# Optimization experiments

Hardware: AMD Instinct MI355X
Metric: run time of the kernel (lower is better)

## Reference

```python
import jax, jax.numpy as jnp
import numpy as np

N, IN_DIM, HIDDEN, OUT_DIM = 16384, 4, 64, 2


def setup_inputs() -> dict:
    key = jax.random.key(0)
    ks = jax.random.split(key, 12)
    x = jax.random.normal(ks[0], (N, IN_DIM), dtype=jnp.float32)
    adj = jax.random.uniform(ks[1], (N, N), dtype=jnp.float32)
    adj = adj / jnp.sum(adj, axis=1, keepdims=True)  # row-normalised
    s = 0.1
    return {
        "x": x,
        "adj": adj,
        # msg_mlp: Linear(4,64) -> Tanh -> Linear(64,64)
        "W1": jax.random.normal(ks[2], (IN_DIM, HIDDEN), dtype=jnp.float32) * s,
        "b1": jnp.zeros((HIDDEN,), dtype=jnp.float32),
        "W2": jax.random.normal(ks[3], (HIDDEN, HIDDEN), dtype=jnp.float32) * s,
        "b2": jnp.zeros((HIDDEN,), dtype=jnp.float32),
        # update_mlp: Linear(68,64) -> Tanh -> Linear(64,64) -> Tanh
        "U1": jax.random.normal(ks[4], (IN_DIM + HIDDEN, HIDDEN), dtype=jnp.float32) * s,
        "c1": jnp.zeros((HIDDEN,), dtype=jnp.float32),
        "U2": jax.random.normal(ks[5], (HIDDEN, HIDDEN), dtype=jnp.float32) * s,
        "c2": jnp.zeros((HIDDEN,), dtype=jnp.float32),
        # out_head: Linear(64,2)
        "Wo": jax.random.normal(ks[6], (HIDDEN, OUT_DIM), dtype=jnp.float32) * s,
        "bo": jnp.zeros((OUT_DIM,), dtype=jnp.float32),
    }


def reference(x, adj, W1, b1, W2, b2, U1, c1, U2, c2, Wo, bo):
    # messages = msg_mlp(x): (N, HIDDEN)
    messages = jnp.tanh(x @ W1 + b1) @ W2 + b2
    # aggregate over neighbours: (N,N) @ (N,HIDDEN)
    agg = adj @ messages
    # combined = [x, agg]: (N, IN_DIM+HIDDEN)
    combined = jnp.concatenate([x, agg], axis=-1)
    h = jnp.tanh(jnp.tanh(combined @ U1 + c1) @ U2 + c2)
    acc = h @ Wo + bo  # (N, OUT_DIM)
    return acc
```

## Files before the change

### kernel.cpp

```cpp
#include <hip/hip_runtime.h>
#include <math.h>

#define NN 16384
#define IN_DIM 4
#define HID 64
#define OUT_DIM 2
#define BK 256
#define NT (NN / BK)

typedef __bf16 bf16x8 __attribute__((ext_vector_type(8)));
typedef float  f32x4  __attribute__((ext_vector_type(4)));

__device__ __forceinline__ void gload_lds16(const float* g, void* lds) {
    __builtin_amdgcn_global_load_lds(
        (const __attribute__((address_space(1))) void*)g,
        (__attribute__((address_space(3))) void*)lds, 16, 0, 0);
}

template<int N> __device__ __forceinline__ void waitv() {
    asm volatile("s_waitcnt vmcnt(%0)" :: "n"(N) : "memory");
    __builtin_amdgcn_sched_barrier(0);
}

__global__ __launch_bounds__(256) void k_messages(
    const float* __restrict__ x, const float* __restrict__ W1,
    const float* __restrict__ b1, const float* __restrict__ W2,
    const float* __restrict__ b2, __bf16* __restrict__ msgT)
{
    __shared__ float  xs[64 * 4];
    __shared__ float  h1[64 * 64];
    __shared__ __bf16 mt[64 * 66];

    const int t = threadIdx.x;
    const int node0 = blockIdx.x * 64;
    xs[t] = x[node0 * 4 + t];
    __syncthreads();

    const int h = t & 63, g = t >> 6;
    for (int n = g * 16; n < g * 16 + 16; ++n) {
        float acc = b1[h];
        #pragma unroll
        for (int k = 0; k < 4; ++k) acc += xs[n * 4 + k] * W1[k * 64 + h];
        h1[n * 64 + h] = tanhf(acc);
    }
    __syncthreads();
    for (int n = g * 16; n < g * 16 + 16; ++n) {
        float acc = b2[h];
        #pragma unroll 8
        for (int k = 0; k < 64; ++k) acc += h1[n * 64 + k] * W2[k * 64 + h];
        mt[h * 66 + n] = (__bf16)acc;
    }
    __syncthreads();
    for (int slot = t; slot < 512; slot += 256) {
        const int r = slot >> 3, c = (slot & 7) * 8;
        bf16x8 v;
        #pragma unroll
        for (int j = 0; j < 8; ++j) v[j] = mt[r * 66 + c + j];
        *(bf16x8*)(msgT + (size_t)r * NN + node0 + c) = v;
    }
}

__global__ __launch_bounds__(128, 1) void k_agg(
    const float* __restrict__ adj, const __bf16* __restrict__ msgT,
    float* __restrict__ agg)
{
    __shared__ float As[2][2][16 * BK];

    const int t = threadIdx.x;
    const int wave = t >> 6, lane = t & 63;
    const int m0 = blockIdx.x * 32 + wave * 16;
    const int r15 = lane & 15;
    const int kg  = lane >> 4;

    const float*  arow  = adj  + (size_t)m0 * NN;
    const __bf16* bbase = msgT + (size_t)r15 * NN + kg * 8;

    float* wbuf0 = &As[0][wave][0];
    float* wbuf1 = &As[1][wave][0];

    f32x4 acc0 = {}, acc1 = {}, acc2 = {}, acc3 = {};
    bf16x8 bc0, bc1, bc2, bc3, bn0, bn1, bn2, bn3;

    #pragma unroll
    for (int g = 0; g < 16; ++g)
        gload_lds16(arow + (size_t)g * NN + ((lane ^ g) << 2), wbuf0 + g * BK);
    bc0 = *(const bf16x8*)(bbase);
    bc1 = *(const bf16x8*)(bbase + 16 * (size_t)NN);
    bc2 = *(const bf16x8*)(bbase + 32 * (size_t)NN);
    bc3 = *(const bf16x8*)(bbase + 48 * (size_t)NN);

#define KSTEP(KT, KK, WAITN, DOSTAGE, DOBN)                                        \
    {                                                                              \
        if (DOBN) {                                                                \
            const int nkt = ((KK) == 7) ? (KT) + 1 : (KT);                         \
            const int nkk = ((KK) + 1) & 7;                                        \
            const __bf16* bp = bbase + (size_t)nkt * BK + nkk * 32;                \
            bn0 = *(const bf16x8*)(bp);                                            \
            bn1 = *(const bf16x8*)(bp + 16 * (size_t)NN);                          \
            bn2 = *(const bf16x8*)(bp + 32 * (size_t)NN);                          \
            bn3 = *(const bf16x8*)(bp + 48 * (size_t)NN);                          \
        }                                                                          \
        if (WAITN) waitv<(WAITN) ? (WAITN) : 63>();                                \
        const float* Ab = (((KT) & 1) ? wbuf1 : wbuf0) + r15 * BK;                 \
        f32x4 alo = *(const f32x4*)(Ab + ((((KK) * 8 + kg * 2 + 0) ^ r15) << 2));  \
        f32x4 ahi = *(const f32x4*)(Ab + ((((KK) * 8 + kg * 2 + 1) ^ r15) << 2));  \
        bf16x8 af;                                                                 \
        af[0] = (__bf16)alo[0]; af[1] = (__bf16)alo[1];                            \
        af[2] = (__bf16)alo[2]; af[3] = (__bf16)alo[3];                            \
        af[4] = (__bf16)ahi[0]; af[5] = (__bf16)ahi[1];                            \
        af[6] = (__bf16)ahi[2]; af[7] = (__bf16)ahi[3];                            \
        acc0 = __builtin_amdgcn_mfma_f32_16x16x32_bf16(af, bc0, acc0, 0, 0, 0);    \
        acc1 = __builtin_amdgcn_mfma_f32_16x16x32_bf16(af, bc1, acc1, 0, 0, 0);    \
        acc2 = __builtin_amdgcn_mfma_f32_16x16x32_bf16(af, bc2, acc2, 0, 0, 0);    \
        acc3 = __builtin_amdgcn_mfma_f32_16x16x32_bf16(af, bc3, acc3, 0, 0, 0);    \
        if (DOSTAGE) {                                                             \
            float* dst = (((KT) & 1) ? wbuf0 : wbuf1);                             \
            _Pragma("unroll")                                                      \
            for (int q = 0; q < 4; ++q) {                                          \
                const int g = (KK) * 4 + q;                                        \
                gload_lds16(arow + (size_t)g * NN + (size_t)((KT) + 1) * BK        \
                                 + ((lane ^ g) << 2), dst + g * BK);               \
            }                                                                      \
        }                                                                          \
        bc0 = bn0; bc1 = bn1; bc2 = bn2; bc3 = bn3;                                \
        __builtin_amdgcn_sched_barrier(0);                                         \
    }

    KSTEP(0, 0, 8, 1, 1);
    #pragma unroll
    for (int kk = 1; kk < 8; ++kk) KSTEP(0, kk, 0, (kk < 4), 1);

    for (int kt = 1; kt < NT - 1; ++kt) {
        KSTEP(kt, 0, 20, 1, 1);
        #pragma unroll
        for (int kk = 1; kk < 8; ++kk) KSTEP(kt, kk, 0, (kk < 4), 1);
    }

    KSTEP((NT - 1), 0, 20, 0, 1);
    #pragma unroll
    for (int kk = 1; kk < 8; ++kk) KSTEP((NT - 1), kk, 0, 0, (kk != 7));
#undef KSTEP

    const int rb = m0 + kg * 4;
    f32x4 accs[4] = {acc0, acc1, acc2, acc3};
    #pragma unroll
    for (int tt = 0; tt < 4; ++tt) {
        #pragma unroll
        for (int j = 0; j < 4; ++j) {
            agg[(size_t)(rb + j) * HID + tt * 16 + r15] = accs[tt][j];
        }
    }
}

__global__ __launch_bounds__(256) void k_update(
    const float* __restrict__ x, const float* __restrict__ agg,
    const float* __restrict__ U1, const float* __restrict__ c1,
    const float* __restrict__ U2, const float* __restrict__ c2,
    const float* __restrict__ Wo, const float* __restrict__ bo,
    float* __restrict__ out)
{
    __shared__ float comb[64 * 73];
    __shared__ float h1s[64 * 66];

    const int t = threadIdx.x, h = t & 63, g = t >> 6;
    const int node0 = blockIdx.x * 64;

    comb[(t >> 2) * 73 + (t & 3)] = x[node0 * 4 + t];
    for (int n = g * 16; n < g * 16 + 16; ++n) {
        comb[n * 73 + 4 + h] = agg[(size_t)(node0 + n) * HID + h];
    }
    __syncthreads();
    for (int n = g * 16; n < g * 16 + 16; ++n) {
        float acc = c1[h];
        #pragma unroll 4
        for (int k = 0; k < 68; ++k) acc += comb[n * 73 + k] * U1[k * 64 + h];
        h1s[n * 66 + h] = tanhf(acc);
    }
    __syncthreads();
    for (int n = g * 16; n < g * 16 + 16; ++n) {
        float acc = c2[h];
        #pragma unroll 8
        for (int k = 0; k < 64; ++k) acc += h1s[n * 66 + k] * U2[k * 64 + h];
        comb[n * 73 + h] = tanhf(acc);
    }
    __syncthreads();
    if (t < 128) {
        const int n = t >> 1, o = t & 1;
        float acc = bo[o];
        #pragma unroll 8
        for (int k = 0; k < 64; ++k) acc += comb[n * 73 + k] * Wo[k * 2 + o];
        out[(size_t)(node0 + n) * 2 + o] = acc;
    }
}

extern "C" void kernel_launch(void* const* d_in, const int* in_sizes, int n_in,
                              void* d_out, int out_size, void* d_ws, size_t ws_size,
                              hipStream_t stream)
{
    const float* x   = (const float*)d_in[0];
    const float* adj = (const float*)d_in[1];
    const float* W1  = (const float*)d_in[2];
    const float* b1  = (const float*)d_in[3];
    const float* W2  = (const float*)d_in[4];
    const float* b2  = (const float*)d_in[5];
    const float* U1  = (const float*)d_in[6];
    const float* c1  = (const float*)d_in[7];
    const float* U2  = (const float*)d_in[8];
    const float* c2  = (const float*)d_in[9];
    const float* Wo  = (const float*)d_in[10];
    const float* bo  = (const float*)d_in[11];
    float* out = (float*)d_out;

    __bf16* msgT = (__bf16*)d_ws;
    float*  agg  = (float*)((char*)d_ws + (size_t)HID * NN * sizeof(__bf16));

    k_messages<<<NN / 64, 256, 0, stream>>>(x, W1, b1, W2, b2, msgT);
    k_agg<<<NN / 32, 128, 0, stream>>>(adj, msgT, agg);
    k_update<<<NN / 64, 256, 0, stream>>>(x, agg, U1, c1, U2, c2, Wo, bo, out);
}
```

Measured before the change: 373.1 us.

## Process paired K-tiles per step and stagger each wave's starting tile

```diff
diff --git a/kernel.cpp b/kernel.cpp
--- a/kernel.cpp
+++ b/kernel.cpp
@@ -6,7 +6,7 @@
 #define HID 64
 #define OUT_DIM 2
 #define BK 256
-#define NT (NN / BK)
+#define NPAIR 32
 
 typedef __bf16 bf16x8 __attribute__((ext_vector_type(8)));
 typedef float  f32x4  __attribute__((ext_vector_type(4)));
@@ -64,81 +64,117 @@
     const float* __restrict__ adj, const __bf16* __restrict__ msgT,
     float* __restrict__ agg)
 {
-    __shared__ float As[2][2][16 * BK];
+    __shared__ float As[2][2][2][16 * BK];
 
     const int t = threadIdx.x;
     const int wave = t >> 6, lane = t & 63;
     const int m0 = blockIdx.x * 32 + wave * 16;
     const int r15 = lane & 15;
     const int kg  = lane >> 4;
+    const int phase = (blockIdx.x * 2 + wave) & (NPAIR - 1);
 
     const float*  arow  = adj  + (size_t)m0 * NN;
     const __bf16* bbase = msgT + (size_t)r15 * NN + kg * 8;
 
-    float* wbuf0 = &As[0][wave][0];
-    float* wbuf1 = &As[1][wave][0];
-
     f32x4 acc0 = {}, acc1 = {}, acc2 = {}, acc3 = {};
-    bf16x8 bc0, bc1, bc2, bc3, bn0, bn1, bn2, bn3;
-
-    #pragma unroll
-    for (int g = 0; g < 16; ++g)
-        gload_lds16(arow + (size_t)g * NN + ((lane ^ g) << 2), wbuf0 + g * BK);
-    bc0 = *(const bf16x8*)(bbase);
-    bc1 = *(const bf16x8*)(bbase + 16 * (size_t)NN);
-    bc2 = *(const bf16x8*)(bbase + 32 * (size_t)NN);
-    bc3 = *(const bf16x8*)(bbase + 48 * (size_t)NN);
-
-#define KSTEP(KT, KK, WAITN, DOSTAGE, DOBN)                                        \
+    bf16x8 bc0, bc1, bc2, bc3, bd0, bd1, bd2, bd3;
+    bf16x8 bn0, bn1, bn2, bn3, bn4, bn5, bn6, bn7;
+
+    {
+        const size_t c0 = (size_t)phase * BK;
+        const size_t c1 = c0 + NPAIR * BK;
+        float* d0 = &As[0][wave][0][0];
+        float* d1 = &As[0][wave][1][0];
+        #pragma unroll
+        for (int gp = 0; gp < 8; ++gp) {
+            const int g = gp * 2;
+            gload_lds16(arow + (size_t)g * NN + c0 + ((lane ^ g) << 2), d0 + g * BK);
+            gload_lds16(arow + (size_t)g * NN + c1 + ((lane ^ g) << 2), d1 + g * BK);
+            gload_lds16(arow + (size_t)(g + 1) * NN + c0 + ((lane ^ (g + 1)) << 2), d0 + (g + 1) * BK);
+            gload_lds16(arow + (size_t)(g + 1) * NN + c1 + ((lane ^ (g + 1)) << 2), d1 + (g + 1) * BK);
+        }
+        const __bf16* bp0 = bbase + (size_t)phase * BK;
+        const __bf16* bp1 = bp0 + (size_t)NPAIR * BK;
+        bc0 = *(const bf16x8*)(bp0);
+        bc1 = *(const bf16x8*)(bp0 + 16 * (size_t)NN);
+        bc2 = *(const bf16x8*)(bp0 + 32 * (size_t)NN);
+        bc3 = *(const bf16x8*)(bp0 + 48 * (size_t)NN);
+        bd0 = *(const bf16x8*)(bp1);
+        bd1 = *(const bf16x8*)(bp1 + 16 * (size_t)NN);
+        bd2 = *(const bf16x8*)(bp1 + 32 * (size_t)NN);
+        bd3 = *(const bf16x8*)(bp1 + 48 * (size_t)NN);
+    }
+
+#define KSTEP(KT, KK, GATE, DOSTAGE, DOBN)                                         \
     {                                                                              \
         if (DOBN) {                                                                \
             const int nkt = ((KK) == 7) ? (KT) + 1 : (KT);                         \
             const int nkk = ((KK) + 1) & 7;                                        \
-            const __bf16* bp = bbase + (size_t)nkt * BK + nkk * 32;                \
-            bn0 = *(const bf16x8*)(bp);                                            \
-            bn1 = *(const bf16x8*)(bp + 16 * (size_t)NN);                          \
-            bn2 = *(const bf16x8*)(bp + 32 * (size_t)NN);                          \
-            bn3 = *(const bf16x8*)(bp + 48 * (size_t)NN);                          \
+            const int npt = (nkt + phase) & (NPAIR - 1);                           \
+            const __bf16* bp0 = bbase + (size_t)npt * BK + nkk * 32;               \
+            const __bf16* bp1 = bp0 + (size_t)NPAIR * BK;                          \
+            bn0 = *(const bf16x8*)(bp0);                                           \
+            bn1 = *(const bf16x8*)(bp0 + 16 * (size_t)NN);                         \
+            bn2 = *(const bf16x8*)(bp0 + 32 * (size_t)NN);                         \
+            bn3 = *(const bf16x8*)(bp0 + 48 * (size_t)NN);                         \
+            bn4 = *(const bf16x8*)(bp1);                                           \
+            bn5 = *(const bf16x8*)(bp1 + 16 * (size_t)NN);                         \
+            bn6 = *(const bf16x8*)(bp1 + 32 * (size_t)NN);                         \
+            bn7 = *(const bf16x8*)(bp1 + 48 * (size_t)NN);                         \
         }                                                                          \
-        if (WAITN) waitv<(WAITN) ? (WAITN) : 63>();                                \
-        const float* Ab = (((KT) & 1) ? wbuf1 : wbuf0) + r15 * BK;                 \
-        f32x4 alo = *(const f32x4*)(Ab + ((((KK) * 8 + kg * 2 + 0) ^ r15) << 2));  \
-        f32x4 ahi = *(const f32x4*)(Ab + ((((KK) * 8 + kg * 2 + 1) ^ r15) << 2));  \
-        bf16x8 af;                                                                 \
-        af[0] = (__bf16)alo[0]; af[1] = (__bf16)alo[1];                            \
-        af[2] = (__bf16)alo[2]; af[3] = (__bf16)alo[3];                            \
-        af[4] = (__bf16)ahi[0]; af[5] = (__bf16)ahi[1];                            \
-        af[6] = (__bf16)ahi[2]; af[7] = (__bf16)ahi[3];                            \
-        acc0 = __builtin_amdgcn_mfma_f32_16x16x32_bf16(af, bc0, acc0, 0, 0, 0);    \
-        acc1 = __builtin_amdgcn_mfma_f32_16x16x32_bf16(af, bc1, acc1, 0, 0, 0);    \
-        acc2 = __builtin_amdgcn_mfma_f32_16x16x32_bf16(af, bc2, acc2, 0, 0, 0);    \
-        acc3 = __builtin_amdgcn_mfma_f32_16x16x32_bf16(af, bc3, acc3, 0, 0, 0);    \
+        if (GATE) waitv<8>();                                                      \
+        const float* A0 = &As[(KT) & 1][wave][0][0] + r15 * BK;                    \
+        const float* A1 = &As[(KT) & 1][wave][1][0] + r15 * BK;                    \
+        f32x4 alo0 = *(const f32x4*)(A0 + ((((KK) * 8 + kg * 2 + 0) ^ r15) << 2)); \
+        f32x4 ahi0 = *(const f32x4*)(A0 + ((((KK) * 8 + kg * 2 + 1) ^ r15) << 2)); \
+        f32x4 alo1 = *(const f32x4*)(A1 + ((((KK) * 8 + kg * 2 + 0) ^ r15) << 2)); \
+        f32x4 ahi1 = *(const f32x4*)(A1 + ((((KK) * 8 + kg * 2 + 1) ^ r15) << 2)); \
+        bf16x8 af0, af1;                                                           \
+        af0[0] = (__bf16)alo0[0]; af0[1] = (__bf16)alo0[1];                        \
+        af0[2] = (__bf16)alo0[2]; af0[3] = (__bf16)alo0[3];                        \
+        af0[4] = (__bf16)ahi0[0]; af0[5] = (__bf16)ahi0[1];                        \
+        af0[6] = (__bf16)ahi0[2]; af0[7] = (__bf16)ahi0[3];                        \
+        af1[0] = (__bf16)alo1[0]; af1[1] = (__bf16)alo1[1];                        \
+        af1[2] = (__bf16)alo1[2]; af1[3] = (__bf16)alo1[3];                        \
+        af1[4] = (__bf16)ahi1[0]; af1[5] = (__bf16)ahi1[1];                        \
+        af1[6] = (__bf16)ahi1[2]; af1[7] = (__bf16)ahi1[3];                        \
+        acc0 = __builtin_amdgcn_mfma_f32_16x16x32_bf16(af0, bc0, acc0, 0, 0, 0);   \
+        acc1 = __builtin_amdgcn_mfma_f32_16x16x32_bf16(af0, bc1, acc1, 0, 0, 0);   \
+        acc2 = __builtin_amdgcn_mfma_f32_16x16x32_bf16(af0, bc2, acc2, 0, 0, 0);   \
+        acc3 = __builtin_amdgcn_mfma_f32_16x16x32_bf16(af0, bc3, acc3, 0, 0, 0);   \
+        acc0 = __builtin_amdgcn_mfma_f32_16x16x32_bf16(af1, bd0, acc0, 0, 0, 0);   \
+        acc1 = __builtin_amdgcn_mfma_f32_16x16x32_bf16(af1, bd1, acc1, 0, 0, 0);   \
+        acc2 = __builtin_amdgcn_mfma_f32_16x16x32_bf16(af1, bd2, acc2, 0, 0, 0);   \
+        acc3 = __builtin_amdgcn_mfma_f32_16x16x32_bf16(af1, bd3, acc3, 0, 0, 0);   \
         if (DOSTAGE) {                                                             \
-            float* dst = (((KT) & 1) ? wbuf0 : wbuf1);                             \
-            _Pragma("unroll")                                                      \
-            for (int q = 0; q < 4; ++q) {                                          \
-                const int g = (KK) * 4 + q;                                        \
-                gload_lds16(arow + (size_t)g * NN + (size_t)((KT) + 1) * BK        \
-                                 + ((lane ^ g) << 2), dst + g * BK);               \
-            }                                                                      \
+            const size_t sc0 = (size_t)(((KT) + 1 + phase) & (NPAIR - 1)) * BK;    \
+            const size_t sc1 = sc0 + NPAIR * BK;                                   \
+            float* d0 = &As[((KT) + 1) & 1][wave][0][0];                           \
+            float* d1 = &As[((KT) + 1) & 1][wave][1][0];                           \
+            const int g = (KK) * 2;                                                \
+            gload_lds16(arow + (size_t)g * NN + sc0 + ((lane ^ g) << 2), d0 + g * BK); \
+            gload_lds16(arow + (size_t)g * NN + sc1 + ((lane ^ g) << 2), d1 + g * BK); \
+            gload_lds16(arow + (size_t)(g + 1) * NN + sc0 + ((lane ^ (g + 1)) << 2), d0 + (g + 1) * BK); \
+            gload_lds16(arow + (size_t)(g + 1) * NN + sc1 + ((lane ^ (g + 1)) << 2), d1 + (g + 1) * BK); \
         }                                                                          \
         bc0 = bn0; bc1 = bn1; bc2 = bn2; bc3 = bn3;                                \
+        bd0 = bn4; bd1 = bn5; bd2 = bn6; bd3 = bn7;                                \
         __builtin_amdgcn_sched_barrier(0);                                         \
     }
 
-    KSTEP(0, 0, 8, 1, 1);
+    KSTEP(0, 0, 1, 1, 1);
     #pragma unroll
-    for (int kk = 1; kk < 8; ++kk) KSTEP(0, kk, 0, (kk < 4), 1);
-
-    for (int kt = 1; kt < NT - 1; ++kt) {
-        KSTEP(kt, 0, 20, 1, 1);
-        #pragma unroll
-        for (int kk = 1; kk < 8; ++kk) KSTEP(kt, kk, 0, (kk < 4), 1);
-    }
-
-    KSTEP((NT - 1), 0, 20, 0, 1);
+    for (int kk = 1; kk < 8; ++kk) KSTEP(0, kk, 0, 1, 1);
+
+    for (int kt = 1; kt < NPAIR - 1; ++kt) {
+        KSTEP(kt, 0, 1, 1, 1);
+        #pragma unroll
+        for (int kk = 1; kk < 8; ++kk) KSTEP(kt, kk, 0, 1, 1);
+    }
+
+    KSTEP((NPAIR - 1), 0, 1, 0, 1);
     #pragma unroll
-    for (int kk = 1; kk < 8; ++kk) KSTEP((NT - 1), kk, 0, 0, (kk != 7));
+    for (int kk = 1; kk < 8; ++kk) KSTEP((NPAIR - 1), kk, 0, 0, (kk != 7));
 #undef KSTEP
 
     const int rb = m0 + kg * 4;
```

Result: slower. 411.6 us (+10.3%).
